# Kernel optimization log

Measured on AMD Instinct MI355X. Metric: run time of the kernel, lower is better.

Reference implementation:

```python
import jax, jax.numpy as jnp
import numpy as np

B = 65536
X_DIM = 362
A = 3  # action_space / number of expert dynamics MLPs


def setup_inputs() -> dict:
    key = jax.random.key(0)
    ks = jax.random.split(key, 12)
    batch_x = jax.random.normal(ks[0], (B, X_DIM), dtype=jnp.float32)
    batch_next = jax.random.normal(ks[1], (B, X_DIM), dtype=jnp.float32)
    # Plant the pointer sentinel (value 10.0) at a random in-bounds grid cell per row,
    # so that ptr-19 >= 0 and ptr+19 < X_DIM (grid width is 19).
    ptr_pos = jax.random.randint(ks[2], (B,), 20, 343)
    batch_x = batch_x.at[jnp.arange(B), ptr_pos].set(10.0)
    batch_a = jax.random.randint(ks[3], (B,), 0, A, dtype=jnp.int32)

    def lin(k, fan_in, shape):
        return (jax.random.normal(k, shape, dtype=jnp.float32) / np.sqrt(fan_in)).astype(jnp.float32)

    W1 = lin(ks[4], 6, (A, 6, 100));   b1 = jnp.zeros((A, 100), jnp.float32)
    W2 = lin(ks[5], 100, (A, 100, 400)); b2 = jnp.zeros((A, 400), jnp.float32)
    W3 = lin(ks[6], 400, (A, 400, 100)); b3 = jnp.zeros((A, 100), jnp.float32)
    W4 = lin(ks[7], 100, (A, 100, 6));  b4 = jnp.zeros((A, 6), jnp.float32)
    return {"batch_x": batch_x, "batch_next": batch_next, "batch_a": batch_a,
            "W1": W1, "b1": b1, "W2": W2, "b2": b2, "W3": W3, "b3": b3, "W4": W4, "b4": b4}


def _attend(data, ptr):
    # cell_list = [0, p, p-19 (left), p+19 (right), p-1 (above), p+1 (below)]
    zeros = jnp.zeros_like(ptr)
    idx = jnp.stack([zeros, ptr, ptr - 19, ptr + 19, ptr - 1, ptr + 1], axis=1)  # [B, 6]
    return jnp.take_along_axis(data, idx, axis=1)  # [B, 6]


def _expert(x, a, W1, b1, W2, b2, W3, b3, W4, b4):
    h = jax.nn.relu(x @ W1[a] + b1[a])
    h = jax.nn.relu(h @ W2[a] + b2[a])
    h = jax.nn.relu(h @ W3[a] + b3[a])
    return h @ W4[a] + b4[a]


def reference(batch_x, batch_next, batch_a, W1, b1, W2, b2, W3, b3, W4, b4):
    # Pointer index = first occurrence of sentinel value 10.0 per row.
    ptr = jnp.argmax(batch_x == 10.0, axis=1)  # [B]
    att = _attend(batch_x, ptr)        # [B, 6]
    att_next = _attend(batch_next, ptr)  # [B, 6]
    # Per-action routed expert MLPs (A is small and fixed): compute each expert
    # over the batch and select per-sample by action id.
    preds = jnp.zeros_like(att)
    for a in range(A):
        out_a = _expert(att, a, W1, b1, W2, b2, W3, b3, W4, b4)
        preds = jnp.where((batch_a == a)[:, None], out_a, preds)
    actual_deltas = att_next - att
    return jnp.mean((preds - actual_deltas) ** 2)
```

## Files before the change

### kernel.cpp

```cpp
#include <hip/hip_runtime.h>
#include <hip/hip_bf16.h>

#define B_ROWS 65536
#define XD 362

typedef __bf16 bf16;
typedef __attribute__((ext_vector_type(8))) __bf16 bf16x8;
typedef __attribute__((ext_vector_type(4))) float f32x4;
typedef __attribute__((ext_vector_type(2))) float f32x2;

#define MFMA16(A, Bf, C) __builtin_amdgcn_mfma_f32_16x16x32_bf16(A, Bf, C, 0, 0, 0)
#define ORDER() __builtin_amdgcn_sched_barrier(0x7F)

#define OFF_W1T   0u
#define OFF_W2T   21504u
#define OFF_W3T   328704u
#define OFF_W4T   608256u
#define OFF_CNT   620544u
#define OFF_PTR   621056u
#define OFF_ATTC  883200u
#define OFF_DELTA 4028928u
#define OFF_PART  8747520u

#define MLP_BX 512
#define WPREP_BLOCKS 600
#define SCAN_BLOCKS 2896

__global__ __launch_bounds__(256) void k_prep(
    const float* __restrict__ W1, const float* __restrict__ b1,
    const float* __restrict__ W2, const float* __restrict__ b2,
    const float* __restrict__ W3, const float* __restrict__ b3,
    const float* __restrict__ W4, const float* __restrict__ b4,
    const float* __restrict__ x,
    bf16* __restrict__ W1t, bf16* __restrict__ W2t,
    bf16* __restrict__ W3t, bf16* __restrict__ W4t,
    int* __restrict__ cnt, int* __restrict__ ptrArr)
{
  int bx = blockIdx.x;
  if (bx >= WPREP_BLOCKS) {
    int gid = (bx - WPREP_BLOCKS) * 256 + threadIdx.x;
    const float4* x4 = (const float4*)x;
#pragma unroll
    for (int u = 0; u < 8; ++u) {
      int i = gid + u * (SCAN_BLOCKS * 256);
      float4 v = x4[i];
      if (v.x == 10.0f || v.y == 10.0f || v.z == 10.0f || v.w == 10.0f) {
        int flat = i * 4;
        if (v.x == 10.0f) ptrArr[(flat    ) / XD] = (flat    ) % XD;
        if (v.y == 10.0f) ptrArr[(flat + 1) / XD] = (flat + 1) % XD;
        if (v.z == 10.0f) ptrArr[(flat + 2) / XD] = (flat + 2) % XD;
        if (v.w == 10.0f) ptrArr[(flat + 3) / XD] = (flat + 3) % XD;
      }
    }
    return;
  }
  int i = bx * 256 + threadIdx.x;
  if (i == 0) { cnt[0] = 0; cnt[1] = 0; cnt[2] = 0; }
  if (i < 3*400*128) {
    int k = i & 127; int rn = i >> 7; int n = rn % 400; int a = rn / 400;
    float v = 0.f;
    if (k < 100) v = W2[(a*100 + k)*400 + n];
    else if (k == 100) v = b2[a*400 + n];
    W2t[i] = (bf16)v;
  }
  if (i < 3*112*416) {
    int k = i % 416; int rn = i / 416; int n = rn % 112; int a = rn / 112;
    float v = 0.f;
    if (n < 100) {
      if (k < 400) v = W3[(a*400 + k)*100 + n];
      else if (k == 400) v = b3[a*100 + n];
    }
    W3t[i] = (bf16)v;
  }
  if (i < 3*112*32) {
    int k = i & 31; int rn = i >> 5; int n = rn % 112; int a = rn / 112;
    float v = 0.f;
    if (n < 100) {
      if (k < 6) v = W1[(a*6 + k)*100 + n];
      else if (k == 6) v = b1[a*100 + n];
    }
    W1t[i] = (bf16)v;
  }
  if (i < 3*16*128) {
    int k = i & 127; int rn = i >> 7; int n = rn & 15; int a = rn >> 4;
    float v = 0.f;
    if (n < 6) {
      if (k < 100) v = W4[(a*100 + k)*6 + n];
      else if (k == 100) v = b4[a*6 + n];
    }
    W4t[i] = (bf16)v;
  }
}

__global__ __launch_bounds__(256) void k_gather2(
    const float* __restrict__ x, const float* __restrict__ xn,
    const int* __restrict__ act, const int* __restrict__ ptrArr,
    bf16* __restrict__ attC, float* __restrict__ deltaC, int* __restrict__ cnt)
{
  int row = blockIdx.x * 256 + threadIdx.x;
  int lane = threadIdx.x & 63;
  int p = ptrArr[row];
  if (p < 20 || p > 342) p = 20;
  const float* xr = x  + (size_t)row * XD;
  const float* nr = xn + (size_t)row * XD;
  int cells[6] = {0, p, p - 19, p + 19, p - 1, p + 1};
  float av[6], dv[6];
#pragma unroll
  for (int i = 0; i < 6; ++i) {
    av[i] = xr[cells[i]];
    dv[i] = nr[cells[i]] - av[i];
  }
  int a = act[row];
  unsigned long long m0 = __ballot(a == 0);
  unsigned long long m1 = __ballot(a == 1);
  unsigned long long m2 = __ballot(a == 2);
  int b0 = 0, b1 = 0, b2 = 0;
  if (lane == 0) {
    b0 = atomicAdd(&cnt[0], (int)__popcll(m0));
    b1 = atomicAdd(&cnt[1], (int)__popcll(m1));
    b2 = atomicAdd(&cnt[2], (int)__popcll(m2));
  }
  b0 = __shfl(b0, 0); b1 = __shfl(b1, 0); b2 = __shfl(b2, 0);
  unsigned long long lt = (1ull << lane) - 1ull;
  unsigned long long ma = (a == 0) ? m0 : (a == 1) ? m1 : m2;
  int base            = (a == 0) ? b0 : (a == 1) ? b1 : b2;
  int slot = base + (int)__popcll(ma & lt);
  size_t rb = (size_t)a * B_ROWS + slot;
  bf16x8 av8;
#pragma unroll
  for (int i = 0; i < 6; ++i) av8[i] = (bf16)av[i];
  av8[6] = (bf16)1.0f;
  av8[7] = (bf16)0.0f;
  *(bf16x8*)(attC + rb * 8) = av8;
  f32x2 d01 = {dv[0], dv[1]}, d23 = {dv[2], dv[3]}, d45 = {dv[4], dv[5]};
  *(f32x2*)(deltaC + rb * 6)     = d01;
  *(f32x2*)(deltaC + rb * 6 + 2) = d23;
  *(f32x2*)(deltaC + rb * 6 + 4) = d45;
}

__global__ __launch_bounds__(256, 2) void k_mlp(
    const bf16* __restrict__ W1t, const bf16* __restrict__ W2t,
    const bf16* __restrict__ W3t, const bf16* __restrict__ W4t,
    const bf16* __restrict__ attC, const float* __restrict__ deltaC,
    const int* __restrict__ cnt, float* __restrict__ partial)
{
  int a = blockIdx.y;
  int count = cnt[a];
  int start = blockIdx.x << 7;
  int pslot = a * MLP_BX + blockIdx.x;
  __shared__ __align__(16) bf16 h1s[4][16][136];
  __shared__ __align__(16) bf16 tr[4][2][16][56];
  __shared__ float s_part[4];
  int wv = threadIdx.x >> 6, lane = threadIdx.x & 63;
  int q = lane >> 4, c = lane & 15;

  if (start < count) {
    const bf16* W1a = W1t + a * 112 * 32;
    const bf16* W2a = W2t + a * 400 * 128;
    const bf16* W3a = W3t + a * 112 * 416;
    const bf16* W4a = W4t + a * 16 * 128;

    for (int i = lane; i < 16 * 16; i += 64)
      h1s[wv][i >> 4][112 + (i & 15)] = (bf16)0.0f;

    bf16x8 A2[2][4];
#pragma unroll
    for (int mi = 0; mi < 2; ++mi) {
      bf16x8 aAtt;
#pragma unroll
      for (int i = 0; i < 8; ++i) aAtt[i] = (bf16)0.0f;
      int slot = start + wv * 32 + mi * 16 + c;
      if (q == 0 && slot < count)
        aAtt = *(const bf16x8*)(attC + ((size_t)a * B_ROWS + slot) * 8);
#pragma unroll
      for (int nt = 0; nt < 7; ++nt) {
        bf16x8 b = *(const bf16x8*)(W1a + (nt * 16 + c) * 32 + q * 8);
        f32x4 C = {0.f, 0.f, 0.f, 0.f};
        C = MFMA16(aAtt, b, C);
        int n = nt * 16 + c;
#pragma unroll
        for (int rg = 0; rg < 4; ++rg) {
          float v = (n < 100) ? (C[rg] > 0.f ? C[rg] : 0.f)
                              : (n == 100 ? 1.0f : 0.0f);
          h1s[wv][q * 4 + rg][n] = (bf16)v;
        }
      }
      ORDER();
#pragma unroll
      for (int tt = 0; tt < 4; ++tt)
        A2[mi][tt] = *(const bf16x8*)&h1s[wv][c][tt * 32 + q * 8];
      ORDER();
    }

    f32x4 C3[2][7];
#pragma unroll
    for (int mi = 0; mi < 2; ++mi)
#pragma unroll
      for (int i = 0; i < 7; ++i) C3[mi][i] = (f32x4){0.f, 0.f, 0.f, 0.f};

#pragma unroll 2
    for (int t = 0; t < 12; ++t) {
      bf16x8 b2f[2][4];
#pragma unroll
      for (int half = 0; half < 2; ++half)
#pragma unroll
        for (int tt = 0; tt < 4; ++tt)
          b2f[half][tt] = *(const bf16x8*)(W2a + ((2*t + half) * 16 + c) * 128 + tt * 32 + q * 8);
#pragma unroll
      for (int mi = 0; mi < 2; ++mi)
#pragma unroll
        for (int half = 0; half < 2; ++half) {
          f32x4 C = {0.f, 0.f, 0.f, 0.f};
#pragma unroll
          for (int tt = 0; tt < 4; ++tt)
            C = MFMA16(A2[mi][tt], b2f[half][tt], C);
#pragma unroll
          for (int rg = 0; rg < 4; ++rg) {
            float v = C[rg] > 0.f ? C[rg] : 0.f;
            tr[wv][mi][q * 4 + rg][half * 16 + c] = (bf16)v;
          }
        }
      ORDER();
      bf16x8 A3a = *(const bf16x8*)&tr[wv][0][c][q * 8];
      bf16x8 A3b = *(const bf16x8*)&tr[wv][1][c][q * 8];
#pragma unroll
      for (int nt3 = 0; nt3 < 7; ++nt3) {
        bf16x8 b = *(const bf16x8*)(W3a + (nt3 * 16 + c) * 416 + t * 32 + q * 8);
        C3[0][nt3] = MFMA16(A3a, b, C3[0][nt3]);
        C3[1][nt3] = MFMA16(A3b, b, C3[1][nt3]);
      }
      ORDER();
    }
    {
      const int t = 12;
      bf16x8 b2f[4];
#pragma unroll
      for (int tt = 0; tt < 4; ++tt)
        b2f[tt] = *(const bf16x8*)(W2a + (24 * 16 + c) * 128 + tt * 32 + q * 8);
#pragma unroll
      for (int mi = 0; mi < 2; ++mi) {
        f32x4 C = {0.f, 0.f, 0.f, 0.f};
#pragma unroll
        for (int tt = 0; tt < 4; ++tt)
          C = MFMA16(A2[mi][tt], b2f[tt], C);
#pragma unroll
        for (int rg = 0; rg < 4; ++rg) {
          float v = C[rg] > 0.f ? C[rg] : 0.f;
          tr[wv][mi][q * 4 + rg][c]      = (bf16)v;
          tr[wv][mi][q * 4 + rg][16 + c] = (bf16)((c == 0) ? 1.0f : 0.0f);
        }
      }
      ORDER();
      bf16x8 A3a = *(const bf16x8*)&tr[wv][0][c][q * 8];
      bf16x8 A3b = *(const bf16x8*)&tr[wv][1][c][q * 8];
#pragma unroll
      for (int nt3 = 0; nt3 < 7; ++nt3) {
        bf16x8 b = *(const bf16x8*)(W3a + (nt3 * 16 + c) * 416 + t * 32 + q * 8);
        C3[0][nt3] = MFMA16(A3a, b, C3[0][nt3]);
        C3[1][nt3] = MFMA16(A3b, b, C3[1][nt3]);
      }
      ORDER();
    }

    bf16x8 b4f[4];
#pragma unroll
    for (int tt = 0; tt < 4; ++tt)
      b4f[tt] = *(const bf16x8*)(W4a + c * 128 + tt * 32 + q * 8);
    float sq = 0.f;
#pragma unroll
    for (int mi = 0; mi < 2; ++mi) {
#pragma unroll
      for (int nt3 = 0; nt3 < 7; ++nt3) {
        int n = nt3 * 16 + c;
#pragma unroll
        for (int rg = 0; rg < 4; ++rg) {
          float v = (n < 100) ? (C3[mi][nt3][rg] > 0.f ? C3[mi][nt3][rg] : 0.f)
                              : (n == 100 ? 1.0f : 0.0f);
          h1s[wv][q * 4 + rg][n] = (bf16)v;
        }
      }
      ORDER();
      f32x4 C4 = {0.f, 0.f, 0.f, 0.f};
#pragma unroll
      for (int tt = 0; tt < 4; ++tt) {
        bf16x8 A4 = *(const bf16x8*)&h1s[wv][c][tt * 32 + q * 8];
        C4 = MFMA16(A4, b4f[tt], C4);
      }
      ORDER();
      if (c < 6) {
#pragma unroll
        for (int rg = 0; rg < 4; ++rg) {
          int slot = start + wv * 32 + mi * 16 + q * 4 + rg;
          if (slot < count) {
            float d = deltaC[((size_t)a * B_ROWS + slot) * 6 + c];
            float e = C4[rg] - d;
            sq += e * e;
          }
        }
      }
    }
#pragma unroll
    for (int off = 32; off; off >>= 1) sq += __shfl_xor(sq, off);
    if (lane == 0) s_part[wv] = sq;
  } else {
    if (lane == 0) s_part[wv] = 0.f;
  }
  __syncthreads();
  if (threadIdx.x == 0)
    partial[pslot] = s_part[0] + s_part[1] + s_part[2] + s_part[3];
}

__global__ __launch_bounds__(256) void k_final(
    const float* __restrict__ partial, float* __restrict__ out)
{
  __shared__ float s[4];
  int t = threadIdx.x, lane = t & 63, wv = t >> 6;
  float sum = 0.f;
  for (int i = t; i < 3 * MLP_BX; i += 256) sum += partial[i];
#pragma unroll
  for (int off = 32; off; off >>= 1) sum += __shfl_xor(sum, off);
  if (lane == 0) s[wv] = sum;
  __syncthreads();
  if (t == 0) {
    double tot = (double)s[0] + s[1] + s[2] + s[3];
    out[0] = (float)(tot / (double)(B_ROWS * 6));
  }
}

extern "C" void kernel_launch(void* const* d_in, const int* in_sizes, int n_in,
                              void* d_out, int out_size, void* d_ws, size_t ws_size,
                              hipStream_t stream)
{
  const float* x  = (const float*)d_in[0];
  const float* xn = (const float*)d_in[1];
  const int*  act = (const int*)d_in[2];
  const float* W1 = (const float*)d_in[3];
  const float* b1 = (const float*)d_in[4];
  const float* W2 = (const float*)d_in[5];
  const float* b2 = (const float*)d_in[6];
  const float* W3 = (const float*)d_in[7];
  const float* b3 = (const float*)d_in[8];
  const float* W4 = (const float*)d_in[9];
  const float* b4 = (const float*)d_in[10];

  char* ws = (char*)d_ws;
  bf16*   W1t    = (bf16*)(ws + OFF_W1T);
  bf16*   W2t    = (bf16*)(ws + OFF_W2T);
  bf16*   W3t    = (bf16*)(ws + OFF_W3T);
  bf16*   W4t    = (bf16*)(ws + OFF_W4T);
  int*    cnt    = (int*)(ws + OFF_CNT);
  int*    ptrArr = (int*)(ws + OFF_PTR);
  bf16*   attC   = (bf16*)(ws + OFF_ATTC);
  float*  deltaC = (float*)(ws + OFF_DELTA);
  float*  part   = (float*)(ws + OFF_PART);

  k_prep<<<dim3(WPREP_BLOCKS + SCAN_BLOCKS), dim3(256), 0, stream>>>(
      W1, b1, W2, b2, W3, b3, W4, b4, x, W1t, W2t, W3t, W4t, cnt, ptrArr);
  k_gather2<<<dim3(B_ROWS / 256), dim3(256), 0, stream>>>(x, xn, act, ptrArr,
                                                          attC, deltaC, cnt);
  k_mlp<<<dim3(MLP_BX, 3), dim3(256), 0, stream>>>(W1t, W2t, W3t, W4t,
                                                   attC, deltaC, cnt, part);
  k_final<<<dim3(1), dim3(256), 0, stream>>>(part, (float*)d_out);
}
```

Before: 296.8 us.

## Flatten expert grid into one compact tile queue and prefetch next weights

The MLP kernel moves from a 512x3 grid, where most blocks exit early, to a 1D grid of 520 blocks that map onto per-expert tiles using prefix sums of the counts. W2 is padded to 416 rows, with the bias-one column folded in, so the last step no longer needs special handling. The layer loop is now uniform: the next W2 fragments and the current W3 fragments are loaded at the top of each iteration, software-pipelined ahead of the MFMAs. The aim is to cut idle-block launch overhead and hide global weight-load latency, at the cost of more live registers, which could reduce occupancy.

```diff
diff --git a/kernel.cpp b/kernel.cpp
--- a/kernel.cpp
+++ b/kernel.cpp
@@ -14,16 +14,16 @@
 
 #define OFF_W1T   0u
 #define OFF_W2T   21504u
-#define OFF_W3T   328704u
-#define OFF_W4T   608256u
-#define OFF_CNT   620544u
-#define OFF_PTR   621056u
-#define OFF_ATTC  883200u
-#define OFF_DELTA 4028928u
-#define OFF_PART  8747520u
-
-#define MLP_BX 512
-#define WPREP_BLOCKS 600
+#define OFF_W3T   340992u
+#define OFF_W4T   620544u
+#define OFF_CNT   632832u
+#define OFF_PTR   633088u
+#define OFF_ATTC  895232u
+#define OFF_DELTA 4040960u
+#define OFF_PART  8759552u
+
+#define MLP_GRID 520
+#define WPREP_BLOCKS 624
 #define SCAN_BLOCKS 2896
 
 __global__ __launch_bounds__(256) void k_prep(
@@ -56,11 +56,15 @@
   }
   int i = bx * 256 + threadIdx.x;
   if (i == 0) { cnt[0] = 0; cnt[1] = 0; cnt[2] = 0; }
-  if (i < 3*400*128) {
-    int k = i & 127; int rn = i >> 7; int n = rn % 400; int a = rn / 400;
+  if (i < 3*416*128) {
+    int k = i & 127; int rn = i >> 7; int n = rn % 416; int a = rn / 416;
     float v = 0.f;
-    if (k < 100) v = W2[(a*100 + k)*400 + n];
-    else if (k == 100) v = b2[a*400 + n];
+    if (n < 400) {
+      if (k < 100) v = W2[(a*100 + k)*400 + n];
+      else if (k == 100) v = b2[a*400 + n];
+    } else if (n == 400) {
+      v = (k == 100) ? 1.0f : 0.0f;
+    }
     W2t[i] = (bf16)v;
   }
   if (i < 3*112*416) {
@@ -144,170 +148,160 @@
     const bf16* __restrict__ attC, const float* __restrict__ deltaC,
     const int* __restrict__ cnt, float* __restrict__ partial)
 {
-  int a = blockIdx.y;
-  int count = cnt[a];
-  int start = blockIdx.x << 7;
-  int pslot = a * MLP_BX + blockIdx.x;
+  int c0 = cnt[0], c1 = cnt[1], c2 = cnt[2];
+  int T0 = (c0 + 127) >> 7, T1 = (c1 + 127) >> 7, T2 = (c2 + 127) >> 7;
+  int b = blockIdx.x;
+  int a, tile, count;
+  if (b < T0)           { a = 0; tile = b;            count = c0; }
+  else if (b < T0 + T1) { a = 1; tile = b - T0;       count = c1; }
+  else if (b < T0 + T1 + T2) { a = 2; tile = b - T0 - T1; count = c2; }
+  else { if (threadIdx.x == 0) partial[b] = 0.f; return; }
+  int start = tile << 7;
+
   __shared__ __align__(16) bf16 h1s[4][16][136];
   __shared__ __align__(16) bf16 tr[4][2][16][56];
   __shared__ float s_part[4];
   int wv = threadIdx.x >> 6, lane = threadIdx.x & 63;
   int q = lane >> 4, c = lane & 15;
 
-  if (start < count) {
-    const bf16* W1a = W1t + a * 112 * 32;
-    const bf16* W2a = W2t + a * 400 * 128;
-    const bf16* W3a = W3t + a * 112 * 416;
-    const bf16* W4a = W4t + a * 16 * 128;
-
-    for (int i = lane; i < 16 * 16; i += 64)
-      h1s[wv][i >> 4][112 + (i & 15)] = (bf16)0.0f;
-
-    bf16x8 A2[2][4];
-#pragma unroll
-    for (int mi = 0; mi < 2; ++mi) {
-      bf16x8 aAtt;
-#pragma unroll
-      for (int i = 0; i < 8; ++i) aAtt[i] = (bf16)0.0f;
-      int slot = start + wv * 32 + mi * 16 + c;
-      if (q == 0 && slot < count)
-        aAtt = *(const bf16x8*)(attC + ((size_t)a * B_ROWS + slot) * 8);
-#pragma unroll
-      for (int nt = 0; nt < 7; ++nt) {
-        bf16x8 b = *(const bf16x8*)(W1a + (nt * 16 + c) * 32 + q * 8);
+  const bf16* W1a = W1t + a * 112 * 32;
+  const bf16* W2a = W2t + a * 416 * 128;
+  const bf16* W3a = W3t + a * 112 * 416;
+  const bf16* W4a = W4t + a * 16 * 128;
+
+  for (int i = lane; i < 16 * 16; i += 64)
+    h1s[wv][i >> 4][112 + (i & 15)] = (bf16)0.0f;
+
+  bf16x8 A2[2][4];
+#pragma unroll
+  for (int mi = 0; mi < 2; ++mi) {
+    bf16x8 aAtt;
+#pragma unroll
+    for (int i = 0; i < 8; ++i) aAtt[i] = (bf16)0.0f;
+    int slot = start + wv * 32 + mi * 16 + c;
+    if (q == 0 && slot < count)
+      aAtt = *(const bf16x8*)(attC + ((size_t)a * B_ROWS + slot) * 8);
+#pragma unroll
+    for (int nt = 0; nt < 7; ++nt) {
+      bf16x8 bw = *(const bf16x8*)(W1a + (nt * 16 + c) * 32 + q * 8);
+      f32x4 C = {0.f, 0.f, 0.f, 0.f};
+      C = MFMA16(aAtt, bw, C);
+      int n = nt * 16 + c;
+#pragma unroll
+      for (int rg = 0; rg < 4; ++rg) {
+        float v = (n < 100) ? (C[rg] > 0.f ? C[rg] : 0.f)
+                            : (n == 100 ? 1.0f : 0.0f);
+        h1s[wv][q * 4 + rg][n] = (bf16)v;
+      }
+    }
+    ORDER();
+#pragma unroll
+    for (int tt = 0; tt < 4; ++tt)
+      A2[mi][tt] = *(const bf16x8*)&h1s[wv][c][tt * 32 + q * 8];
+    ORDER();
+  }
+
+  f32x4 C3[2][7];
+#pragma unroll
+  for (int mi = 0; mi < 2; ++mi)
+#pragma unroll
+    for (int i = 0; i < 7; ++i) C3[mi][i] = (f32x4){0.f, 0.f, 0.f, 0.f};
+
+  bf16x8 b2f[2][4];
+#pragma unroll
+  for (int half = 0; half < 2; ++half)
+#pragma unroll
+    for (int tt = 0; tt < 4; ++tt)
+      b2f[half][tt] = *(const bf16x8*)(W2a + (half * 16 + c) * 128 + tt * 32 + q * 8);
+
+#pragma unroll 1
+  for (int t = 0; t < 13; ++t) {
+    bf16x8 w3f[7];
+#pragma unroll
+    for (int nt3 = 0; nt3 < 7; ++nt3)
+      w3f[nt3] = *(const bf16x8*)(W3a + (nt3 * 16 + c) * 416 + t * 32 + q * 8);
+    int tn = (t < 12) ? t + 1 : 12;
+    bf16x8 b2n[2][4];
+#pragma unroll
+    for (int half = 0; half < 2; ++half)
+#pragma unroll
+      for (int tt = 0; tt < 4; ++tt)
+        b2n[half][tt] = *(const bf16x8*)(W2a + ((2 * tn + half) * 16 + c) * 128 + tt * 32 + q * 8);
+    __builtin_amdgcn_sched_barrier(0);
+
+#pragma unroll
+    for (int mi = 0; mi < 2; ++mi)
+#pragma unroll
+      for (int half = 0; half < 2; ++half) {
         f32x4 C = {0.f, 0.f, 0.f, 0.f};
-        C = MFMA16(aAtt, b, C);
-        int n = nt * 16 + c;
-#pragma unroll
-        for (int rg = 0; rg < 4; ++rg) {
-          float v = (n < 100) ? (C[rg] > 0.f ? C[rg] : 0.f)
-                              : (n == 100 ? 1.0f : 0.0f);
-          h1s[wv][q * 4 + rg][n] = (bf16)v;
-        }
-      }
-      ORDER();
-#pragma unroll
-      for (int tt = 0; tt < 4; ++tt)
-        A2[mi][tt] = *(const bf16x8*)&h1s[wv][c][tt * 32 + q * 8];
-      ORDER();
-    }
-
-    f32x4 C3[2][7];
-#pragma unroll
-    for (int mi = 0; mi < 2; ++mi)
-#pragma unroll
-      for (int i = 0; i < 7; ++i) C3[mi][i] = (f32x4){0.f, 0.f, 0.f, 0.f};
-
-#pragma unroll 2
-    for (int t = 0; t < 12; ++t) {
-      bf16x8 b2f[2][4];
-#pragma unroll
-      for (int half = 0; half < 2; ++half)
 #pragma unroll
         for (int tt = 0; tt < 4; ++tt)
-          b2f[half][tt] = *(const bf16x8*)(W2a + ((2*t + half) * 16 + c) * 128 + tt * 32 + q * 8);
-#pragma unroll
-      for (int mi = 0; mi < 2; ++mi)
-#pragma unroll
-        for (int half = 0; half < 2; ++half) {
-          f32x4 C = {0.f, 0.f, 0.f, 0.f};
-#pragma unroll
-          for (int tt = 0; tt < 4; ++tt)
-            C = MFMA16(A2[mi][tt], b2f[half][tt], C);
-#pragma unroll
-          for (int rg = 0; rg < 4; ++rg) {
-            float v = C[rg] > 0.f ? C[rg] : 0.f;
-            tr[wv][mi][q * 4 + rg][half * 16 + c] = (bf16)v;
-          }
-        }
-      ORDER();
-      bf16x8 A3a = *(const bf16x8*)&tr[wv][0][c][q * 8];
-      bf16x8 A3b = *(const bf16x8*)&tr[wv][1][c][q * 8];
-#pragma unroll
-      for (int nt3 = 0; nt3 < 7; ++nt3) {
-        bf16x8 b = *(const bf16x8*)(W3a + (nt3 * 16 + c) * 416 + t * 32 + q * 8);
-        C3[0][nt3] = MFMA16(A3a, b, C3[0][nt3]);
-        C3[1][nt3] = MFMA16(A3b, b, C3[1][nt3]);
-      }
-      ORDER();
-    }
-    {
-      const int t = 12;
-      bf16x8 b2f[4];
-#pragma unroll
-      for (int tt = 0; tt < 4; ++tt)
-        b2f[tt] = *(const bf16x8*)(W2a + (24 * 16 + c) * 128 + tt * 32 + q * 8);
-#pragma unroll
-      for (int mi = 0; mi < 2; ++mi) {
-        f32x4 C = {0.f, 0.f, 0.f, 0.f};
-#pragma unroll
-        for (int tt = 0; tt < 4; ++tt)
-          C = MFMA16(A2[mi][tt], b2f[tt], C);
+          C = MFMA16(A2[mi][tt], b2f[half][tt], C);
 #pragma unroll
         for (int rg = 0; rg < 4; ++rg) {
           float v = C[rg] > 0.f ? C[rg] : 0.f;
-          tr[wv][mi][q * 4 + rg][c]      = (bf16)v;
-          tr[wv][mi][q * 4 + rg][16 + c] = (bf16)((c == 0) ? 1.0f : 0.0f);
+          tr[wv][mi][q * 4 + rg][half * 16 + c] = (bf16)v;
         }
       }
-      ORDER();
-      bf16x8 A3a = *(const bf16x8*)&tr[wv][0][c][q * 8];
-      bf16x8 A3b = *(const bf16x8*)&tr[wv][1][c][q * 8];
-#pragma unroll
-      for (int nt3 = 0; nt3 < 7; ++nt3) {
-        bf16x8 b = *(const bf16x8*)(W3a + (nt3 * 16 + c) * 416 + t * 32 + q * 8);
-        C3[0][nt3] = MFMA16(A3a, b, C3[0][nt3]);
-        C3[1][nt3] = MFMA16(A3b, b, C3[1][nt3]);
-      }
-      ORDER();
-    }
-
-    bf16x8 b4f[4];
-#pragma unroll
-    for (int tt = 0; tt < 4; ++tt)
-      b4f[tt] = *(const bf16x8*)(W4a + c * 128 + tt * 32 + q * 8);
-    float sq = 0.f;
-#pragma unroll
-    for (int mi = 0; mi < 2; ++mi) {
-#pragma unroll
-      for (int nt3 = 0; nt3 < 7; ++nt3) {
-        int n = nt3 * 16 + c;
-#pragma unroll
-        for (int rg = 0; rg < 4; ++rg) {
-          float v = (n < 100) ? (C3[mi][nt3][rg] > 0.f ? C3[mi][nt3][rg] : 0.f)
-                              : (n == 100 ? 1.0f : 0.0f);
-          h1s[wv][q * 4 + rg][n] = (bf16)v;
+    ORDER();
+    bf16x8 A3a = *(const bf16x8*)&tr[wv][0][c][q * 8];
+    bf16x8 A3b = *(const bf16x8*)&tr[wv][1][c][q * 8];
+#pragma unroll
+    for (int nt3 = 0; nt3 < 7; ++nt3) {
+      C3[0][nt3] = MFMA16(A3a, w3f[nt3], C3[0][nt3]);
+      C3[1][nt3] = MFMA16(A3b, w3f[nt3], C3[1][nt3]);
+    }
+    ORDER();
+#pragma unroll
+    for (int half = 0; half < 2; ++half)
+#pragma unroll
+      for (int tt = 0; tt < 4; ++tt)
+        b2f[half][tt] = b2n[half][tt];
+  }
+
+  bf16x8 b4f[4];
+#pragma unroll
+  for (int tt = 0; tt < 4; ++tt)
+    b4f[tt] = *(const bf16x8*)(W4a + c * 128 + tt * 32 + q * 8);
+  float sq = 0.f;
+#pragma unroll
+  for (int mi = 0; mi < 2; ++mi) {
+#pragma unroll
+    for (int nt3 = 0; nt3 < 7; ++nt3) {
+      int n = nt3 * 16 + c;
+#pragma unroll
+      for (int rg = 0; rg < 4; ++rg) {
+        float v = (n < 100) ? (C3[mi][nt3][rg] > 0.f ? C3[mi][nt3][rg] : 0.f)
+                            : (n == 100 ? 1.0f : 0.0f);
+        h1s[wv][q * 4 + rg][n] = (bf16)v;
+      }
+    }
+    ORDER();
+    f32x4 C4 = {0.f, 0.f, 0.f, 0.f};
+#pragma unroll
+    for (int tt = 0; tt < 4; ++tt) {
+      bf16x8 A4 = *(const bf16x8*)&h1s[wv][c][tt * 32 + q * 8];
+      C4 = MFMA16(A4, b4f[tt], C4);
+    }
+    ORDER();
+    if (c < 6) {
+#pragma unroll
+      for (int rg = 0; rg < 4; ++rg) {
+        int slot = start + wv * 32 + mi * 16 + q * 4 + rg;
+        if (slot < count) {
+          float d = deltaC[((size_t)a * B_ROWS + slot) * 6 + c];
+          float e = C4[rg] - d;
+          sq += e * e;
         }
       }
-      ORDER();
-      f32x4 C4 = {0.f, 0.f, 0.f, 0.f};
-#pragma unroll
-      for (int tt = 0; tt < 4; ++tt) {
-        bf16x8 A4 = *(const bf16x8*)&h1s[wv][c][tt * 32 + q * 8];
-        C4 = MFMA16(A4, b4f[tt], C4);
-      }
-      ORDER();
-      if (c < 6) {
-#pragma unroll
-        for (int rg = 0; rg < 4; ++rg) {
-          int slot = start + wv * 32 + mi * 16 + q * 4 + rg;
-          if (slot < count) {
-            float d = deltaC[((size_t)a * B_ROWS + slot) * 6 + c];
-            float e = C4[rg] - d;
-            sq += e * e;
-          }
-        }
-      }
-    }
-#pragma unroll
-    for (int off = 32; off; off >>= 1) sq += __shfl_xor(sq, off);
-    if (lane == 0) s_part[wv] = sq;
-  } else {
-    if (lane == 0) s_part[wv] = 0.f;
-  }
+    }
+  }
+#pragma unroll
+  for (int off = 32; off; off >>= 1) sq += __shfl_xor(sq, off);
+  if (lane == 0) s_part[wv] = sq;
   __syncthreads();
   if (threadIdx.x == 0)
-    partial[pslot] = s_part[0] + s_part[1] + s_part[2] + s_part[3];
+    partial[b] = s_part[0] + s_part[1] + s_part[2] + s_part[3];
 }
 
 __global__ __launch_bounds__(256) void k_final(
@@ -316,7 +310,7 @@
   __shared__ float s[4];
   int t = threadIdx.x, lane = t & 63, wv = t >> 6;
   float sum = 0.f;
-  for (int i = t; i < 3 * MLP_BX; i += 256) sum += partial[i];
+  for (int i = t; i < MLP_GRID; i += 256) sum += partial[i];
 #pragma unroll
   for (int off = 32; off; off >>= 1) sum += __shfl_xor(sum, off);
   if (lane == 0) s[wv] = sum;
@@ -358,7 +352,7 @@
       W1, b1, W2, b2, W3, b3, W4, b4, x, W1t, W2t, W3t, W4t, cnt, ptrArr);
   k_gather2<<<dim3(B_ROWS / 256), dim3(256), 0, stream>>>(x, xn, act, ptrArr,
                                                           attC, deltaC, cnt);
-  k_mlp<<<dim3(MLP_BX, 3), dim3(256), 0, stream>>>(W1t, W2t, W3t, W4t,
-                                                   attC, deltaC, cnt, part);
+  k_mlp<<<dim3(MLP_GRID), dim3(256), 0, stream>>>(W1t, W2t, W3t, W4t,
+                                                  attC, deltaC, cnt, part);
   k_final<<<dim3(1), dim3(256), 0, stream>>>(part, (float*)d_out);
 }
```

Result: no change. 296.0 us (-0.3%).
